# Kernel tuning notes

Hardware: AMD Instinct MI355X
Metric: run time of the kernel (lower is better)

## Reference

```python
import jax, jax.numpy as jnp
import numpy as np

EPS = 1e-8

def elu_feature_map(x):
    return jax.nn.elu(x) + 1.0

def setup_inputs() -> dict:
    key = jax.random.key(0)
    ks = jax.random.split(key, 5)
    B, S, D = 2, 4096, 1024
    scale = 1.0 / np.sqrt(D).astype(np.float32)
    x = jax.random.normal(ks[0], (B, S, D), dtype=jnp.float32)
    Wq = jax.random.normal(ks[1], (D, D), dtype=jnp.float32) * scale
    Wk = jax.random.normal(ks[2], (D, D), dtype=jnp.float32) * scale
    Wv = jax.random.normal(ks[3], (D, D), dtype=jnp.float32) * scale
    Wo = jax.random.normal(ks[4], (D, D), dtype=jnp.float32) * scale
    return {"x": x, "Wq": Wq, "Wk": Wk, "Wv": Wv, "Wo": Wo}

def reference(x, Wq, Wk, Wv, Wo):
    B, S, D = x.shape
    H = 16
    Dh = D // H
    # projections (nn.Linear with no bias: x @ W.T)
    def proj(W):
        return (x @ W.T).reshape(B, S, H, Dh)
    q = elu_feature_map(proj(Wq))  # [B,S,H,Dh]
    k = elu_feature_map(proj(Wk))
    v = proj(Wv)
    # scan over sequence: carry running kv_sum [B,H,Dh,Dh] and k_sum [B,H,Dh]
    q_t = jnp.moveaxis(q, 1, 0)  # [S,B,H,Dh]
    k_t = jnp.moveaxis(k, 1, 0)
    v_t = jnp.moveaxis(v, 1, 0)

    def step(carry, qkv):
        kv_sum, k_sum = carry
        q_i, k_i, v_i = qkv  # each [B,H,Dh]
        kv_sum = kv_sum + jnp.einsum('bhd,bhe->bhde', k_i, v_i)
        k_sum = k_sum + k_i
        num = jnp.einsum('bhd,bhde->bhe', q_i, kv_sum)
        den = jnp.sum(q_i * k_sum, axis=-1, keepdims=True)
        out_i = num / (den + EPS)
        return (kv_sum, k_sum), out_i

    kv0 = jnp.zeros((B, H, Dh, Dh), dtype=x.dtype)
    ks0 = jnp.zeros((B, H, Dh), dtype=x.dtype)
    _, out = jax.lax.scan(step, (kv0, ks0), (q_t, k_t, v_t))  # out: [S,B,H,Dh]
    out = jnp.moveaxis(out, 0, 1).reshape(B, S, D)
    return out @ Wo.T
```

## Files before the change

kernel.cpp:

```cpp
#include <hip/hip_runtime.h>
#include <math.h>


#define EPSF 1e-8f

typedef unsigned short u16;
typedef unsigned int   u32;
typedef __attribute__((ext_vector_type(8))) short short8v;
typedef __attribute__((ext_vector_type(4))) float f32x4;

__device__ __forceinline__ float elu1(float x){ return x > 0.f ? x + 1.f : __expf(x); }
__device__ __forceinline__ u16 f2bf(float f){
    union{float f; u32 i;} c; c.f = f;
    u32 i = c.i + 0x7FFFu + ((c.i >> 16) & 1u);
    return (u16)(i >> 16);
}
__device__ __forceinline__ float bflo(u32 v){ union{u32 i; float f;} c; c.i = v << 16; return c.f; }
__device__ __forceinline__ float bfhi(u32 v){ union{u32 i; float f;} c; c.i = v & 0xffff0000u; return c.f; }
__device__ __forceinline__ void f4a(float4 v, float* a){ a[0]=v.x; a[1]=v.y; a[2]=v.z; a[3]=v.w; }

__device__ __forceinline__ void gload16(const void* g, void* l){
    __builtin_amdgcn_global_load_lds((const __attribute__((address_space(1))) u32*)g,
                                     (__attribute__((address_space(3))) u32*)l, 16, 0, 0);
}

__global__ __launch_bounds__(256) void k_cast5(
    const float* __restrict__ x,  const float* __restrict__ wq,
    const float* __restrict__ wk, const float* __restrict__ wv,
    const float* __restrict__ wo,
    u16* __restrict__ xb, u16* __restrict__ wcat, u16* __restrict__ wob)
{
    size_t i8 = ((size_t)blockIdx.x * 256 + threadIdx.x) * 8;
    const float* s; u16* d; size_t off;
    if      (i8 <  8388608) { s = x;  d = xb;            off = i8; }
    else if (i8 <  9437184) { s = wq; d = wcat;          off = i8 - 8388608; }
    else if (i8 < 10485760) { s = wk; d = wcat + 1048576; off = i8 - 9437184; }
    else if (i8 < 11534336) { s = wv; d = wcat + 2097152; off = i8 - 10485760; }
    else                    { s = wo; d = wob;           off = i8 - 11534336; }
    float4 a = *(const float4*)&s[off];
    float4 b = *(const float4*)&s[off + 4];
    uint4 p;
    p.x = (u32)f2bf(a.x) | ((u32)f2bf(a.y) << 16);
    p.y = (u32)f2bf(a.z) | ((u32)f2bf(a.w) << 16);
    p.z = (u32)f2bf(b.x) | ((u32)f2bf(b.y) << 16);
    p.w = (u32)f2bf(b.z) | ((u32)f2bf(b.w) << 16);
    *(uint4*)&d[off] = p;
}

__global__ __launch_bounds__(256) void k_gemm_qkv(
    const u16* __restrict__ A, const u16* __restrict__ W, u16* __restrict__ C)
{
    const int id  = blockIdx.x;
    const int nid = (id & 7) * 192 + (id >> 3);
    const int bx  = nid / 24;
    const int by  = nid % 24;
    const int matrix = by >> 3;
    const bool do_elu = matrix < 2;
    u16* out = C + (size_t)matrix * 8388608;
    const int m0 = bx * 128;
    const int n0 = by * 128;
    const int col0 = (by & 7) * 128;

    __shared__ __align__(16) u16 As[128 * 32];
    __shared__ __align__(16) u16 Bs[128 * 32];
    const int tid = threadIdx.x;
    const int l   = tid & 63;
    const int wv  = tid >> 6;
    const int wr  = (wv >> 1) * 64;
    const int wc  = (wv & 1) * 64;
    const int srow  = tid >> 2;
    const int skoff = (tid & 3) * 8;

    f32x4 acc[4][4];
    #pragma unroll
    for (int m = 0; m < 4; ++m)
        #pragma unroll
        for (int n = 0; n < 4; ++n) acc[m][n] = (f32x4){0.f, 0.f, 0.f, 0.f};

    for (int kt = 0; kt < 1024; kt += 32) {
        __syncthreads();
        #pragma unroll
        for (int h = 0; h < 2; ++h)
            gload16(&A[(size_t)(m0 + h*64 + srow) * 1024 + kt + skoff],
                    (char*)As + h*4096 + wv*1024);
        #pragma unroll
        for (int h = 0; h < 2; ++h)
            gload16(&W[(size_t)(n0 + h*64 + srow) * 1024 + kt + skoff],
                    (char*)Bs + h*4096 + wv*1024);
        __syncthreads();

        short8v a[4], b[4];
        #pragma unroll
        for (int m = 0; m < 4; ++m)
            a[m] = *(const short8v*)&As[(wr + m*16 + (l & 15)) * 32 + (l >> 4) * 8];
        #pragma unroll
        for (int n = 0; n < 4; ++n)
            b[n] = *(const short8v*)&Bs[(wc + n*16 + (l & 15)) * 32 + (l >> 4) * 8];
        #pragma unroll
        for (int m = 0; m < 4; ++m)
            #pragma unroll
            for (int n = 0; n < 4; ++n)
                acc[m][n] = __builtin_amdgcn_mfma_f32_16x16x32_bf16(a[m], b[n], acc[m][n], 0, 0, 0);
    }

    const int r0 = m0 + wr + (l >> 4) * 4;
    const int c0 = col0 + wc + (l & 15);
    #pragma unroll
    for (int m = 0; m < 4; ++m)
        #pragma unroll
        for (int n = 0; n < 4; ++n)
            #pragma unroll
            for (int r = 0; r < 4; ++r) {
                float v = acc[m][n][r];
                if (do_elu) v = elu1(v);
                out[(size_t)(r0 + m*16 + r) * 1024 + c0 + n*16] = f2bf(v);
            }
}

__global__ __launch_bounds__(256) void k_gemm_out(
    const u16* __restrict__ A, const u16* __restrict__ W, float* __restrict__ C)
{
    const int id  = blockIdx.x;
    const int nid = (id & 7) * 64 + (id >> 3);
    const int bx  = nid >> 3;
    const int by  = nid & 7;
    const int m0 = bx * 128;
    const int n0 = by * 128;

    __shared__ __align__(16) u16 As[128 * 32];
    __shared__ __align__(16) u16 Bs[128 * 32];
    const int tid = threadIdx.x;
    const int l   = tid & 63;
    const int wv  = tid >> 6;
    const int wr  = (wv >> 1) * 64;
    const int wc  = (wv & 1) * 64;
    const int srow  = tid >> 2;
    const int skoff = (tid & 3) * 8;

    f32x4 acc[4][4];
    #pragma unroll
    for (int m = 0; m < 4; ++m)
        #pragma unroll
        for (int n = 0; n < 4; ++n) acc[m][n] = (f32x4){0.f, 0.f, 0.f, 0.f};

    for (int kt = 0; kt < 1024; kt += 32) {
        __syncthreads();
        #pragma unroll
        for (int h = 0; h < 2; ++h)
            gload16(&A[(size_t)(m0 + h*64 + srow) * 1024 + kt + skoff],
                    (char*)As + h*4096 + wv*1024);
        #pragma unroll
        for (int h = 0; h < 2; ++h)
            gload16(&W[(size_t)(n0 + h*64 + srow) * 1024 + kt + skoff],
                    (char*)Bs + h*4096 + wv*1024);
        __syncthreads();

        short8v a[4], b[4];
        #pragma unroll
        for (int m = 0; m < 4; ++m)
            a[m] = *(const short8v*)&As[(wr + m*16 + (l & 15)) * 32 + (l >> 4) * 8];
        #pragma unroll
        for (int n = 0; n < 4; ++n)
            b[n] = *(const short8v*)&Bs[(wc + n*16 + (l & 15)) * 32 + (l >> 4) * 8];
        #pragma unroll
        for (int m = 0; m < 4; ++m)
            #pragma unroll
            for (int n = 0; n < 4; ++n)
                acc[m][n] = __builtin_amdgcn_mfma_f32_16x16x32_bf16(a[m], b[n], acc[m][n], 0, 0, 0);
    }

    const int r0 = m0 + wr + (l >> 4) * 4;
    const int c0 = n0 + wc + (l & 15);
    #pragma unroll
    for (int m = 0; m < 4; ++m)
        #pragma unroll
        for (int n = 0; n < 4; ++n)
            #pragma unroll
            for (int r = 0; r < 4; ++r)
                C[(size_t)(r0 + m*16 + r) * 1024 + c0 + n*16] = acc[m][n][r];
}

__global__ __launch_bounds__(256) void k_chunksums(
    const u16* __restrict__ Kg, const u16* __restrict__ Vg,
    float* __restrict__ CKVt, float* __restrict__ CKS)
{
    const int tid = threadIdx.x;
    const int tx = tid & 15, ty = tid >> 4;
    const int c  = blockIdx.x & 63;
    const int bh = blockIdx.x >> 6;
    const int b = bh >> 4, h = bh & 15;
    const int row0 = b * 4096 + c * 64;
    const int col  = h * 64;

    __shared__ float Ks[64][68];
    __shared__ float Vs[64][68];

    #pragma unroll
    for (int r = 0; r < 2; ++r) {
        int idx = tid + r * 256;
        int i = idx >> 3, cg = (idx & 7) << 3;
        uint4 ku = *(const uint4*)&Kg[(size_t)(row0 + i) * 1024 + col + cg];
        uint4 vu = *(const uint4*)&Vg[(size_t)(row0 + i) * 1024 + col + cg];
        Ks[i][cg+0]=bflo(ku.x); Ks[i][cg+1]=bfhi(ku.x);
        Ks[i][cg+2]=bflo(ku.y); Ks[i][cg+3]=bfhi(ku.y);
        Ks[i][cg+4]=bflo(ku.z); Ks[i][cg+5]=bfhi(ku.z);
        Ks[i][cg+6]=bflo(ku.w); Ks[i][cg+7]=bfhi(ku.w);
        Vs[i][cg+0]=bflo(vu.x); Vs[i][cg+1]=bfhi(vu.x);
        Vs[i][cg+2]=bflo(vu.y); Vs[i][cg+3]=bfhi(vu.y);
        Vs[i][cg+4]=bflo(vu.z); Vs[i][cg+5]=bfhi(vu.z);
        Vs[i][cg+6]=bflo(vu.w); Vs[i][cg+7]=bfhi(vu.w);
    }
    __syncthreads();

    float acc[4][4] = {};
    #pragma unroll 8
    for (int i = 0; i < 64; ++i) {
        float kv[4], vv[4];
        f4a(*(const float4*)&Ks[i][ty*4], kv);
        f4a(*(const float4*)&Vs[i][tx*4], vv);
        #pragma unroll
        for (int a = 0; a < 4; ++a)
            #pragma unroll
            for (int e = 0; e < 4; ++e)
                acc[a][e] = fmaf(kv[a], vv[e], acc[a][e]);
    }
    float* ckv = &CKVt[(size_t)blockIdx.x * 4096];
    #pragma unroll
    for (int e = 0; e < 4; ++e)
        *(float4*)&ckv[(tx*4 + e) * 64 + ty*4] =
            make_float4(acc[0][e], acc[1][e], acc[2][e], acc[3][e]);

    if (tid < 64) {
        float s = 0.f;
        #pragma unroll 8
        for (int i = 0; i < 64; ++i) s += Ks[i][tid];
        CKS[(size_t)blockIdx.x * 64 + tid] = s;
    }
}

__global__ __launch_bounds__(256) void k_prefix_kv(
    const float* __restrict__ CKVt, u16* __restrict__ CKVp)
{
    const int bh = blockIdx.x >> 4;
    const int p  = ((blockIdx.x & 15) << 8) + threadIdx.x;
    const size_t base = (size_t)bh * 64 * 4096 + p;
    float acc = 0.f;
    #pragma unroll
    for (int c = 0; c < 64; ++c) {
        float t = CKVt[base + (size_t)c * 4096];
        CKVp[base + (size_t)c * 4096] = f2bf(acc);
        acc += t;
    }
}

__global__ __launch_bounds__(256) void k_prefix_ks(float* __restrict__ CKS)
{
    const int idx = blockIdx.x * 256 + threadIdx.x;
    const int bh = idx >> 6, d = idx & 63;
    const size_t base = (size_t)bh * 64 * 64 + d;
    float v[64];
    #pragma unroll
    for (int c = 0; c < 64; ++c) v[c] = CKS[base + (size_t)c * 64];
    float acc = 0.f;
    #pragma unroll
    for (int c = 0; c < 64; ++c) { float t = v[c]; CKS[base + (size_t)c * 64] = acc; acc += t; }
}

#define LSTR 72
__global__ __launch_bounds__(256) void k_attn2(
    const u16* __restrict__ Qg, const u16* __restrict__ Kg, const u16* __restrict__ Vg,
    const u16* __restrict__ Stg,
    const float* __restrict__ KSg,
    u16* __restrict__ AO)
{
    const int tid = threadIdx.x;
    const int l = tid & 63;
    const int w = tid >> 6;
    const int c  = blockIdx.x & 63;
    const int bh = blockIdx.x >> 6;
    const int row0 = (bh >> 4) * 4096 + c * 64;
    const int col  = (bh & 15) * 64;

    __shared__ __align__(16) u16 Qs [64 * LSTR];
    __shared__ __align__(16) u16 Ks [64 * LSTR];
    __shared__ __align__(16) u16 Vt [64 * LSTR];
    __shared__ __align__(16) u16 Sts[64 * LSTR];
    __shared__ __align__(16) u16 Pl [64 * LSTR];
    __shared__ float ksumF[64];
    __shared__ float invdenL[64];

    #pragma unroll
    for (int r = 0; r < 2; ++r) {
        int idx = tid + r * 256;
        int i = idx >> 3, cg = (idx & 7) << 3;
        *(uint4*)&Qs [i*LSTR + cg] = *(const uint4*)&Qg [(size_t)(row0 + i) * 1024 + col + cg];
        *(uint4*)&Ks [i*LSTR + cg] = *(const uint4*)&Kg [(size_t)(row0 + i) * 1024 + col + cg];
        *(uint4*)&Sts[i*LSTR + cg] = *(const uint4*)&Stg[(size_t)blockIdx.x * 4096 + i * 64 + cg];
        uint4 vu = *(const uint4*)&Vg[(size_t)(row0 + i) * 1024 + col + cg];
        Vt[(cg+0)*LSTR + i] = (u16)(vu.x & 0xffff);
        Vt[(cg+1)*LSTR + i] = (u16)(vu.x >> 16);
        Vt[(cg+2)*LSTR + i] = (u16)(vu.y & 0xffff);
        Vt[(cg+3)*LSTR + i] = (u16)(vu.y >> 16);
        Vt[(cg+4)*LSTR + i] = (u16)(vu.z & 0xffff);
        Vt[(cg+5)*LSTR + i] = (u16)(vu.z >> 16);
        Vt[(cg+6)*LSTR + i] = (u16)(vu.w & 0xffff);
        Vt[(cg+7)*LSTR + i] = (u16)(vu.w >> 16);
    }
    if (tid < 64) ksumF[tid] = KSg[(size_t)blockIdx.x * 64 + tid];
    __syncthreads();

    const int li = l & 15;
    const int lg = l >> 4;
    const int i_row = w * 16 + li;

    short8v bq[2];
    #pragma unroll
    for (int kc = 0; kc < 2; ++kc)
        bq[kc] = *(const short8v*)&Qs[i_row * LSTR + lg*8 + kc*32];

    float den = EPSF;
    #pragma unroll
    for (int mj = 0; mj < 4; ++mj) {
        f32x4 sacc = (f32x4){0.f, 0.f, 0.f, 0.f};
        #pragma unroll
        for (int kc = 0; kc < 2; ++kc) {
            short8v ak = *(const short8v*)&Ks[(mj*16 + li) * LSTR + lg*8 + kc*32];
            sacc = __builtin_amdgcn_mfma_f32_16x16x32_bf16(ak, bq[kc], sacc, 0, 0, 0);
        }
        const int jbase = mj*16 + lg*4;
        float pv[4];
        #pragma unroll
        for (int r = 0; r < 4; ++r) {
            float v = sacc[r];
            v = (jbase + r <= i_row - w*16 + w*16) ? v : 0.f;
            v = (jbase + r <= i_row) ? v : 0.f;
            den += v;
            pv[r] = v;
        }
        u32 lo = (u32)f2bf(pv[0]) | ((u32)f2bf(pv[1]) << 16);
        u32 hi = (u32)f2bf(pv[2]) | ((u32)f2bf(pv[3]) << 16);
        *(uint2*)&Pl[i_row * LSTR + jbase] = make_uint2(lo, hi);
    }

    {
        const int d0 = lg * 16;
        uint4 q1 = *(const uint4*)&Qs[i_row * LSTR + d0];
        uint4 q2 = *(const uint4*)&Qs[i_row * LSTR + d0 + 8];
        den += bflo(q1.x)*ksumF[d0+0] + bfhi(q1.x)*ksumF[d0+1]
             + bflo(q1.y)*ksumF[d0+2] + bfhi(q1.y)*ksumF[d0+3]
             + bflo(q1.z)*ksumF[d0+4] + bfhi(q1.z)*ksumF[d0+5]
             + bflo(q1.w)*ksumF[d0+6] + bfhi(q1.w)*ksumF[d0+7]
             + bflo(q2.x)*ksumF[d0+8] + bfhi(q2.x)*ksumF[d0+9]
             + bflo(q2.y)*ksumF[d0+10]+ bfhi(q2.y)*ksumF[d0+11]
             + bflo(q2.z)*ksumF[d0+12]+ bfhi(q2.z)*ksumF[d0+13]
             + bflo(q2.w)*ksumF[d0+14]+ bfhi(q2.w)*ksumF[d0+15];
    }
    den += __shfl_xor(den, 16);
    den += __shfl_xor(den, 32);
    if (l < 16) invdenL[w*16 + l] = 1.f / den;

    f32x4 oacc[4];
    #pragma unroll
    for (int ne = 0; ne < 4; ++ne) oacc[ne] = (f32x4){0.f, 0.f, 0.f, 0.f};
    #pragma unroll
    for (int kc = 0; kc < 2; ++kc) {
        short8v ap = *(const short8v*)&Pl[i_row * LSTR + lg*8 + kc*32];
        short8v aq = bq[kc];
        #pragma unroll
        for (int ne = 0; ne < 4; ++ne) {
            short8v bv = *(const short8v*)&Vt [(ne*16 + li) * LSTR + lg*8 + kc*32];
            short8v bs = *(const short8v*)&Sts[(ne*16 + li) * LSTR + lg*8 + kc*32];
            oacc[ne] = __builtin_amdgcn_mfma_f32_16x16x32_bf16(ap, bv, oacc[ne], 0, 0, 0);
            oacc[ne] = __builtin_amdgcn_mfma_f32_16x16x32_bf16(aq, bs, oacc[ne], 0, 0, 0);
        }
    }

    float inv[4];
    #pragma unroll
    for (int r = 0; r < 4; ++r) inv[r] = invdenL[w*16 + lg*4 + r];
    #pragma unroll
    for (int ne = 0; ne < 4; ++ne)
        #pragma unroll
        for (int r = 0; r < 4; ++r)
            Pl[(w*16 + lg*4 + r) * LSTR + ne*16 + li] = f2bf(oacc[ne][r] * inv[r]);

    #pragma unroll
    for (int p = 0; p < 2; ++p) {
        int idx2 = l + p * 64;
        int ro = w*16 + (idx2 >> 3), cg = (idx2 & 7) << 3;
        *(uint4*)&AO[(size_t)(row0 + ro) * 1024 + col + cg] = *(const uint4*)&Pl[ro*LSTR + cg];
    }
}

extern "C" void kernel_launch(void* const* d_in, const int* in_sizes, int n_in,
                              void* d_out, int out_size, void* d_ws, size_t ws_size,
                              hipStream_t stream)
{
    const float* x  = (const float*)d_in[0];
    const float* Wq = (const float*)d_in[1];
    const float* Wk = (const float*)d_in[2];
    const float* Wv = (const float*)d_in[3];
    const float* Wo = (const float*)d_in[4];
    float* out = (float*)d_out;

    char* w = (char*)d_ws;
    u16*   QKVb = (u16*)(w);
    u16*   Qb   = QKVb;
    u16*   Kb   = QKVb + 8388608;
    u16*   Vb   = QKVb + 16777216;
    u16*   xb   = (u16*)(w + 50331648);
    u16*   AOb  = xb;
    u16*   Wcat = (u16*)(w + 67108864);
    u16*   Wob  = (u16*)(w + 73400320);
    float* CKV  = (float*)(w + 75497472);
    u16*   CKVp = (u16*)(w + 109051904);
    float* CKS  = (float*)(w + 125829120);

    k_cast5    <<<6144, 256, 0, stream>>>(x, Wq, Wk, Wv, Wo, xb, Wcat, Wob);
    k_gemm_qkv <<<1536, 256, 0, stream>>>(xb, Wcat, QKVb);
    k_chunksums<<<2048, 256, 0, stream>>>(Kb, Vb, CKV, CKS);
    k_prefix_kv<<<512,  256, 0, stream>>>(CKV, CKVp);
    k_prefix_ks<<<8,    256, 0, stream>>>(CKS);
    k_attn2    <<<2048, 256, 0, stream>>>(Qb, Kb, Vb, CKVp, CKS, AOb);
    k_gemm_out <<<512,  256, 0, stream>>>(AOb, Wob, out);
}
```

Baseline: 156.1 us.

## Replace QKV and output GEMMs with pipelined 128x256 swizzled-LDS GEMM kernel

New measurement: 142.6 us. -8.7%, faster.

```diff
diff --git a/kernel.cpp b/kernel.cpp
--- a/kernel.cpp
+++ b/kernel.cpp
@@ -47,29 +47,60 @@
     *(uint4*)&d[off] = p;
 }
 
-__global__ __launch_bounds__(256) void k_gemm_qkv(
-    const u16* __restrict__ A, const u16* __restrict__ W, u16* __restrict__ C)
-{
-    const int id  = blockIdx.x;
-    const int nid = (id & 7) * 192 + (id >> 3);
-    const int bx  = nid / 24;
-    const int by  = nid % 24;
-    const int matrix = by >> 3;
-    const bool do_elu = matrix < 2;
-    u16* out = C + (size_t)matrix * 8388608;
-    const int m0 = bx * 128;
-    const int n0 = by * 128;
-    const int col0 = (by & 7) * 128;
-
-    __shared__ __align__(16) u16 As[128 * 32];
-    __shared__ __align__(16) u16 Bs[128 * 32];
+#define AOFF(BUF,KH) ((BUF)*49152 + (KH)*8192)
+#define BOFF(BUF,KH) ((BUF)*49152 + 16384 + (KH)*16384)
+
+#define ST(BUF, KT, KH) { \
+    gload16(Ag + (size_t)(m0 + sRow)*1024 + (KT)*64 + (KH)*32 + sKg, dsm + AOFF(BUF,KH) + wvv*1024); \
+    gload16(Wg + (size_t)(n0 + sRow)*1024 + (KT)*64 + (KH)*32 + sKg, dsm + BOFF(BUF,KH) + wvv*1024); \
+    gload16(Wg + (size_t)(n0 + 128 + sRow)*1024 + (KT)*64 + (KH)*32 + sKg, dsm + BOFF(BUF,KH) + 8192 + wvv*1024); }
+
+#define PH(BUF, KH, STCODE, CNT) { \
+    short8v a[4], b[4]; \
+    const char* Ab = dsm + AOFF(BUF,KH); \
+    const char* Bb = dsm + BOFF(BUF,KH); \
+    _Pragma("unroll") for (int m = 0; m < 4; ++m) a[m] = *(const short8v*)(Ab + offA[m]); \
+    _Pragma("unroll") for (int n = 0; n < 4; ++n) b[n] = *(const short8v*)(Bb + offB[n]); \
+    STCODE; \
+    __builtin_amdgcn_s_setprio(1); \
+    _Pragma("unroll") for (int m = 0; m < 4; ++m) \
+        _Pragma("unroll") for (int n = 0; n < 4; ++n) \
+            acc[m][n] = __builtin_amdgcn_mfma_f32_16x16x32_bf16(a[m], b[n], acc[m][n], 0, 0, 0); \
+    __builtin_amdgcn_s_setprio(0); \
+    asm volatile("s_waitcnt vmcnt(" #CNT ")" ::: "memory"); \
+    __builtin_amdgcn_s_barrier(); }
+
+template<int MODE, int NBY>
+__global__ __launch_bounds__(512, 2) void k_gemm5(
+    const u16* __restrict__ Ag, const u16* __restrict__ Wg, void* __restrict__ Cv)
+{
+    extern __shared__ char dsm[];
+    const int nid = (blockIdx.x & 7) * ((64 * NBY) >> 3) + (blockIdx.x >> 3);
+    const int bx  = nid / NBY;
+    const int by  = nid % NBY;
+    const int m0  = bx * 128;
+    const int n0  = by * 256;
+
     const int tid = threadIdx.x;
     const int l   = tid & 63;
-    const int wv  = tid >> 6;
-    const int wr  = (wv >> 1) * 64;
-    const int wc  = (wv & 1) * 64;
-    const int srow  = tid >> 2;
-    const int skoff = (tid & 3) * 8;
+    const int wid = tid >> 6;
+    const int wm  = wid >> 2;
+    const int wn  = wid & 3;
+    const int li  = l & 15;
+    const int kgi = l >> 4;
+
+    int offA[4], offB[4];
+    #pragma unroll
+    for (int m = 0; m < 4; ++m) {
+        int ra = wm*64 + m*16 + li;
+        offA[m] = (ra >> 1)*128 + (((((ra & 1) << 2) | kgi) ^ ((ra >> 1) & 7)) << 4);
+        int rb = wn*64 + m*16 + li;
+        offB[m] = (rb >> 1)*128 + (((((rb & 1) << 2) | kgi) ^ ((rb >> 1) & 7)) << 4);
+    }
+    const int wvv  = wid;
+    const int sx   = (l & 7) ^ (l >> 3);
+    const int sRow = 2*(wvv*8 + (l >> 3)) + (sx >> 2);
+    const int sKg  = (sx & 3) * 8;
 
     f32x4 acc[4][4];
     #pragma unroll
@@ -77,25 +108,29 @@
         #pragma unroll
         for (int n = 0; n < 4; ++n) acc[m][n] = (f32x4){0.f, 0.f, 0.f, 0.f};
 
-    for (int kt = 0; kt < 1024; kt += 32) {
-        __syncthreads();
-        #pragma unroll
-        for (int h = 0; h < 2; ++h)
-            gload16(&A[(size_t)(m0 + h*64 + srow) * 1024 + kt + skoff],
-                    (char*)As + h*4096 + wv*1024);
-        #pragma unroll
-        for (int h = 0; h < 2; ++h)
-            gload16(&W[(size_t)(n0 + h*64 + srow) * 1024 + kt + skoff],
-                    (char*)Bs + h*4096 + wv*1024);
-        __syncthreads();
-
+    ST(0, 0, 0); ST(0, 0, 1); ST(1, 1, 0);
+    asm volatile("s_waitcnt vmcnt(6)" ::: "memory");
+    __builtin_amdgcn_s_barrier();
+
+    #pragma unroll 1
+    for (int it = 0; it < 7; ++it) {
+        const int T = it * 2;
+        PH(0, 0, ST(1, T+1, 1), 6);
+        PH(0, 1, ST(0, T+2, 0), 6);
+        PH(1, 0, ST(0, T+2, 1), 6);
+        PH(1, 1, ST(1, T+3, 0), 6);
+    }
+    PH(0, 0, ST(1, 15, 1), 6);
+    PH(0, 1, {}, 3);
+    PH(1, 0, {}, 0);
+    {
         short8v a[4], b[4];
-        #pragma unroll
-        for (int m = 0; m < 4; ++m)
-            a[m] = *(const short8v*)&As[(wr + m*16 + (l & 15)) * 32 + (l >> 4) * 8];
-        #pragma unroll
-        for (int n = 0; n < 4; ++n)
-            b[n] = *(const short8v*)&Bs[(wc + n*16 + (l & 15)) * 32 + (l >> 4) * 8];
+        const char* Ab = dsm + AOFF(1,1);
+        const char* Bb = dsm + BOFF(1,1);
+        #pragma unroll
+        for (int m = 0; m < 4; ++m) a[m] = *(const short8v*)(Ab + offA[m]);
+        #pragma unroll
+        for (int n = 0; n < 4; ++n) b[n] = *(const short8v*)(Bb + offB[n]);
         #pragma unroll
         for (int m = 0; m < 4; ++m)
             #pragma unroll
@@ -103,81 +138,33 @@
                 acc[m][n] = __builtin_amdgcn_mfma_f32_16x16x32_bf16(a[m], b[n], acc[m][n], 0, 0, 0);
     }
 
-    const int r0 = m0 + wr + (l >> 4) * 4;
-    const int c0 = col0 + wc + (l & 15);
-    #pragma unroll
-    for (int m = 0; m < 4; ++m)
-        #pragma unroll
-        for (int n = 0; n < 4; ++n)
-            #pragma unroll
-            for (int r = 0; r < 4; ++r) {
-                float v = acc[m][n][r];
-                if (do_elu) v = elu1(v);
-                out[(size_t)(r0 + m*16 + r) * 1024 + c0 + n*16] = f2bf(v);
-            }
-}
-
-__global__ __launch_bounds__(256) void k_gemm_out(
-    const u16* __restrict__ A, const u16* __restrict__ W, float* __restrict__ C)
-{
-    const int id  = blockIdx.x;
-    const int nid = (id & 7) * 64 + (id >> 3);
-    const int bx  = nid >> 3;
-    const int by  = nid & 7;
-    const int m0 = bx * 128;
-    const int n0 = by * 128;
-
-    __shared__ __align__(16) u16 As[128 * 32];
-    __shared__ __align__(16) u16 Bs[128 * 32];
-    const int tid = threadIdx.x;
-    const int l   = tid & 63;
-    const int wv  = tid >> 6;
-    const int wr  = (wv >> 1) * 64;
-    const int wc  = (wv & 1) * 64;
-    const int srow  = tid >> 2;
-    const int skoff = (tid & 3) * 8;
-
-    f32x4 acc[4][4];
-    #pragma unroll
-    for (int m = 0; m < 4; ++m)
-        #pragma unroll
-        for (int n = 0; n < 4; ++n) acc[m][n] = (f32x4){0.f, 0.f, 0.f, 0.f};
-
-    for (int kt = 0; kt < 1024; kt += 32) {
-        __syncthreads();
-        #pragma unroll
-        for (int h = 0; h < 2; ++h)
-            gload16(&A[(size_t)(m0 + h*64 + srow) * 1024 + kt + skoff],
-                    (char*)As + h*4096 + wv*1024);
-        #pragma unroll
-        for (int h = 0; h < 2; ++h)
-            gload16(&W[(size_t)(n0 + h*64 + srow) * 1024 + kt + skoff],
-                    (char*)Bs + h*4096 + wv*1024);
-        __syncthreads();
-
-        short8v a[4], b[4];
-        #pragma unroll
-        for (int m = 0; m < 4; ++m)
-            a[m] = *(const short8v*)&As[(wr + m*16 + (l & 15)) * 32 + (l >> 4) * 8];
-        #pragma unroll
-        for (int n = 0; n < 4; ++n)
-            b[n] = *(const short8v*)&Bs[(wc + n*16 + (l & 15)) * 32 + (l >> 4) * 8];
+    const int r0 = m0 + wm*64 + (l >> 4) * 4;
+    if (MODE == 1) {
+        const int matrix = by >> 2;
+        const bool do_elu = matrix < 2;
+        u16* out = (u16*)Cv + (size_t)matrix * 8388608;
+        const int c0 = (by & 3) * 256 + wn*64 + li;
         #pragma unroll
         for (int m = 0; m < 4; ++m)
             #pragma unroll
             for (int n = 0; n < 4; ++n)
-                acc[m][n] = __builtin_amdgcn_mfma_f32_16x16x32_bf16(a[m], b[n], acc[m][n], 0, 0, 0);
-    }
-
-    const int r0 = m0 + wr + (l >> 4) * 4;
-    const int c0 = n0 + wc + (l & 15);
-    #pragma unroll
-    for (int m = 0; m < 4; ++m)
-        #pragma unroll
-        for (int n = 0; n < 4; ++n)
+                #pragma unroll
+                for (int r = 0; r < 4; ++r) {
+                    float v = acc[m][n][r];
+                    if (do_elu) v = elu1(v);
+                    out[(size_t)(r0 + m*16 + r) * 1024 + c0 + n*16] = f2bf(v);
+                }
+    } else {
+        float* out = (float*)Cv;
+        const int c0 = n0 + wn*64 + li;
+        #pragma unroll
+        for (int m = 0; m < 4; ++m)
             #pragma unroll
-            for (int r = 0; r < 4; ++r)
-                C[(size_t)(r0 + m*16 + r) * 1024 + c0 + n*16] = acc[m][n][r];
+            for (int n = 0; n < 4; ++n)
+                #pragma unroll
+                for (int r = 0; r < 4; ++r)
+                    out[(size_t)(r0 + m*16 + r) * 1024 + c0 + n*16] = acc[m][n][r];
+    }
 }
 
 __global__ __launch_bounds__(256) void k_chunksums(
@@ -269,9 +256,7 @@
 #define LSTR 72
 __global__ __launch_bounds__(256) void k_attn2(
     const u16* __restrict__ Qg, const u16* __restrict__ Kg, const u16* __restrict__ Vg,
-    const u16* __restrict__ Stg,
-    const float* __restrict__ KSg,
-    u16* __restrict__ AO)
+    const u16* __restrict__ Stg, const float* __restrict__ KSg, u16* __restrict__ AO)
 {
     const int tid = threadIdx.x;
     const int l = tid & 63;
@@ -332,7 +317,6 @@
         #pragma unroll
         for (int r = 0; r < 4; ++r) {
             float v = sacc[r];
-            v = (jbase + r <= i_row - w*16 + w*16) ? v : 0.f;
             v = (jbase + r <= i_row) ? v : 0.f;
             den += v;
             pv[r] = v;
@@ -416,11 +400,16 @@
     u16*   CKVp = (u16*)(w + 109051904);
     float* CKS  = (float*)(w + 125829120);
 
-    k_cast5    <<<6144, 256, 0, stream>>>(x, Wq, Wk, Wv, Wo, xb, Wcat, Wob);
-    k_gemm_qkv <<<1536, 256, 0, stream>>>(xb, Wcat, QKVb);
-    k_chunksums<<<2048, 256, 0, stream>>>(Kb, Vb, CKV, CKS);
-    k_prefix_kv<<<512,  256, 0, stream>>>(CKV, CKVp);
-    k_prefix_ks<<<8,    256, 0, stream>>>(CKS);
-    k_attn2    <<<2048, 256, 0, stream>>>(Qb, Kb, Vb, CKVp, CKS, AOb);
-    k_gemm_out <<<512,  256, 0, stream>>>(AOb, Wob, out);
-}
+    hipFuncSetAttribute(reinterpret_cast<const void*>(k_gemm5<1,12>),
+                        hipFuncAttributeMaxDynamicSharedMemorySize, 98304);
+    hipFuncSetAttribute(reinterpret_cast<const void*>(k_gemm5<3,4>),
+                        hipFuncAttributeMaxDynamicSharedMemorySize, 98304);
+
+    k_cast5      <<<6144, 256, 0, stream>>>(x, Wq, Wk, Wv, Wo, xb, Wcat, Wob);
+    k_gemm5<1,12><<<768,  512, 98304, stream>>>(xb, Wcat, (void*)QKVb);
+    k_chunksums  <<<2048, 256, 0, stream>>>(Kb, Vb, CKV, CKS);
+    k_prefix_kv  <<<512,  256, 0, stream>>>(CKV, CKVp);
+    k_prefix_ks  <<<8,    256, 0, stream>>>(CKS);
+    k_attn2      <<<2048, 256, 0, stream>>>(Qb, Kb, Vb, CKVp, CKS, AOb);
+    k_gemm5<3,4> <<<256,  512, 98304, stream>>>(AOb, Wob, (void*)out);
+}
```
